# Kernel optimization log

Measured on AMD Instinct MI355X. Metric: run time of the kernel, lower is better.

Reference implementation:

```python
import jax, jax.numpy as jnp
import numpy as np

B, T, N, F = 16, 12, 1024, 128
H, DH, C = 8, 16, 64  # heads, d_head (=d_core//H), core_num; note d_in must equal H*DH
EPS = 1e-5


def setup_inputs() -> dict:
    key = jax.random.key(0)
    ks = jax.random.split(key, 12)
    s = lambda fan_in: 1.0 / np.sqrt(fan_in)
    return {
        "input": jax.random.normal(ks[0], (B, T, N, F), jnp.float32),
        # value Linear(d_in,d_in); weights stored [in,out]
        "W_v": jax.random.normal(ks[1], (F, F), jnp.float32) * s(F),
        "b_v": jax.random.normal(ks[2], (F,), jnp.float32) * s(F),
        # core decomposition params
        "adaptive": jax.random.normal(ks[3], (H, DH, N), jnp.float32),
        "cores": jax.random.normal(ks[4], (H, C, DH), jnp.float32),
        # FFN: Linear(2F -> 8F), GELU, Linear(8F -> F)
        "W1": jax.random.normal(ks[5], (2 * F, 8 * F), jnp.float32) * s(2 * F),
        "b1": jax.random.normal(ks[6], (8 * F,), jnp.float32) * s(2 * F),
        "W2": jax.random.normal(ks[7], (8 * F, F), jnp.float32) * s(8 * F),
        "b2": jax.random.normal(ks[8], (F,), jnp.float32) * s(8 * F),
        # BatchNorm2d(d_in) affine params (training-mode batch stats)
        "gamma": jnp.ones((F,), jnp.float32),
        "beta": jnp.zeros((F,), jnp.float32),
    }


def reference(input, W_v, b_v, adaptive, cores, W1, b1, W2, b2, gamma, beta):
    b, t, n, f = input.shape
    h, dh, _ = adaptive.shape
    # value projection, split heads: [b,t,n,f] -> [b,t,h,dh,n]
    v = input @ W_v + b_v
    v = v.reshape(b, t, n, h, dh).transpose(0, 1, 3, 4, 2)
    # core affinity scores [h,c,n]
    aff = jnp.einsum("hcd,hdn->hcn", cores, adaptive) / np.sqrt(dh)
    a_n2c = jax.nn.softmax(aff, axis=-1)  # softmax over nodes
    a_c2n = jax.nn.softmax(aff, axis=-2)  # softmax over cores
    # two-stage aggregation through cores
    v = jnp.einsum("bthfn,hcn->bthfc", v, a_n2c)
    v = jnp.einsum("bthfc,hcn->bthfn", v, a_c2n)
    # merge heads: [b,t,h,dh,n] -> [b,t,f,n] -> [b,t,n,f]
    v = v.reshape(b, t, f, n).swapaxes(-1, -2)
    # FFN on concat([input - v, v]) (dropout off in eval), residual
    x = jnp.concatenate([input - v, v], axis=-1)
    x = jax.nn.gelu(x @ W1 + b1, approximate=False) @ W2 + b2
    out = x + input
    # BatchNorm2d over channel f (batch stats over b,t,n; biased variance)
    mean = out.mean(axis=(0, 1, 2))
    var = out.var(axis=(0, 1, 2))
    return (out - mean) * jax.lax.rsqrt(var + EPS) * gamma + beta
```

## Files before the change

kernel.cpp:

```cpp
#include <hip/hip_runtime.h>
#include <math.h>

#define BB 16
#define TT 12
#define NN 1024
#define FF 128
#define BT 192
#define BTN 196608
#define CNT ((float)BTN)
#define T1SZ 1572864

typedef unsigned short ushort_t;
typedef __attribute__((ext_vector_type(8))) short bf16x8;
typedef __attribute__((ext_vector_type(4))) float f32x4;

__device__ __forceinline__ ushort_t f2bf(float x) {
    union { float f; unsigned u; } c; c.f = x;
    unsigned r = c.u + 0x7fffu + ((c.u >> 16) & 1u);
    return (ushort_t)(r >> 16);
}
__device__ __forceinline__ float bf2f(ushort_t u) {
    union { unsigned u32; float f; } c; c.u32 = ((unsigned)u) << 16; return c.f;
}
__device__ __forceinline__ unsigned pk2(float a, float b) {
    unsigned r;
    asm("v_cvt_pk_bf16_f32 %0, %1, %2" : "=v"(r) : "v"(a), "v"(b));
    return r;
}
__device__ __forceinline__ float gelu_f(float x) {
    float u = x * x;
    float s = x * fmaf(u, -0.10294428f, -2.30220852f);
    float e = __builtin_amdgcn_exp2f(s);
    return x * __builtin_amdgcn_rcpf(1.0f + e);
}

__device__ __forceinline__ char* swz256(void* base, int row, int byteoff) {
    return (char*)base + row * 256 + (byteoff ^ ((row & 7) << 4));
}

__global__ __launch_bounds__(256) void k_sm_n(const float* __restrict__ cores,
                                              const float* __restrict__ adaptive,
                                              float* __restrict__ aff,
                                              ushort_t* __restrict__ out) {
    int row = blockIdx.x;
    int h = row >> 6;
    int t = threadIdx.x;
    __shared__ float red[8];
    const float* cp = cores + row * 16;
    const float* ap = adaptive + h * 16384;
    float v0 = 0.f, v1 = 0.f, v2 = 0.f, v3 = 0.f;
#pragma unroll
    for (int d = 0; d < 16; ++d) {
        float c = cp[d];
        const float* an = ap + d * 1024;
        v0 = fmaf(c, an[t], v0);
        v1 = fmaf(c, an[t + 256], v1);
        v2 = fmaf(c, an[t + 512], v2);
        v3 = fmaf(c, an[t + 768], v3);
    }
    v0 *= 0.25f; v1 *= 0.25f; v2 *= 0.25f; v3 *= 0.25f;
    aff[row * 1024 + t]       = v0;
    aff[row * 1024 + t + 256] = v1;
    aff[row * 1024 + t + 512] = v2;
    aff[row * 1024 + t + 768] = v3;
    float m = fmaxf(fmaxf(v0, v1), fmaxf(v2, v3));
#pragma unroll
    for (int off = 32; off >= 1; off >>= 1) m = fmaxf(m, __shfl_xor(m, off));
    if ((t & 63) == 0) red[t >> 6] = m;
    __syncthreads();
    m = fmaxf(fmaxf(red[0], red[1]), fmaxf(red[2], red[3]));
    v0 = expf(v0 - m); v1 = expf(v1 - m); v2 = expf(v2 - m); v3 = expf(v3 - m);
    float s = v0 + v1 + v2 + v3;
#pragma unroll
    for (int off = 32; off >= 1; off >>= 1) s += __shfl_xor(s, off);
    __syncthreads();
    if ((t & 63) == 0) red[4 + (t >> 6)] = s;
    __syncthreads();
    s = red[4] + red[5] + red[6] + red[7];
    float inv = 1.0f / s;
    out[row * 1024 + t]       = f2bf(v0 * inv);
    out[row * 1024 + t + 256] = f2bf(v1 * inv);
    out[row * 1024 + t + 512] = f2bf(v2 * inv);
    out[row * 1024 + t + 768] = f2bf(v3 * inv);
}

__global__ __launch_bounds__(256) void k_prep(const float* __restrict__ aff,
                                              const float* __restrict__ Wv,
                                              const float* __restrict__ W1,
                                              const float* __restrict__ W2,
                                              ushort_t* __restrict__ a_c2nT,
                                              ushort_t* __restrict__ WvT,
                                              ushort_t* __restrict__ W1f,
                                              ushort_t* __restrict__ W2f,
                                              float* __restrict__ bn_sum) {
    __shared__ __align__(16) char smem[64 * 65 * 4];
    int b = blockIdx.x;
    int t = threadIdx.x;
    if (b < 128) {
        ushort_t (*tile)[72] = (ushort_t(*)[72])smem;
        int h = b >> 4, n0 = (b & 15) * 64;
        int nl = t >> 2, q = t & 3;
        const float* p = aff + h * 65536 + n0 + nl;
        float v[16];
        float m = -1e30f;
#pragma unroll
        for (int i = 0; i < 16; ++i) {
            v[i] = p[(q * 16 + i) * 1024];
            m = fmaxf(m, v[i]);
        }
        m = fmaxf(m, __shfl_xor(m, 1));
        m = fmaxf(m, __shfl_xor(m, 2));
        float s = 0.f;
#pragma unroll
        for (int i = 0; i < 16; ++i) { v[i] = expf(v[i] - m); s += v[i]; }
        s += __shfl_xor(s, 1);
        s += __shfl_xor(s, 2);
        float inv = 1.0f / s;
#pragma unroll
        for (int i = 0; i < 16; ++i) tile[nl][q * 16 + i] = f2bf(v[i] * inv);
        __syncthreads();
        ushort_t* ob = a_c2nT + ((size_t)h * 1024 + n0) * 64;
        for (int i = t; i < 512; i += 256) {
            int r = i >> 3, cq = i & 7;
            *(bf16x8*)&ob[r * 64 + cq * 8] = *(bf16x8*)&tile[r][cq * 8];
        }
    } else if (b < 132) {
        float (*tile)[65] = (float(*)[65])smem;
        int q = b - 128;
        int r0 = (q >> 1) * 64, c0 = (q & 1) * 64;
        for (int i = t; i < 4096; i += 256) {
            int r = i >> 6, c = i & 63;
            tile[r][c] = Wv[(size_t)(r0 + r) * 128 + c0 + c];
        }
        __syncthreads();
        for (int i = t; i < 4096; i += 256) {
            int c = i >> 6, r = i & 63;
            WvT[(size_t)(c0 + c) * 128 + r0 + r] = f2bf(tile[r][c]);
        }
    } else if (b < 260) {
        int tid = (b - 132) * 256 + t;
        int lane = tid & 63, jn = (tid >> 6) & 1, kk = (tid >> 7) & 7;
        int w = (tid >> 10) & 3, ch = tid >> 12;
        int lr = lane & 15, lg = lane >> 4;
        int n = ch * 128 + w * 32 + jn * 16 + lr;
        int kb = kk * 32 + lg * 8;
        ushort_t o[8];
#pragma unroll
        for (int e = 0; e < 8; ++e) o[e] = f2bf(W1[(size_t)(kb + e) * 1024 + n]);
        *(bf16x8*)&W1f[(size_t)tid * 8] = *(bf16x8*)o;
    } else if (b < 324) {
        int tid = (b - 260) * 256 + t;
        int lane = tid & 63, jy = (tid >> 6) & 1, kk = (tid >> 7) & 3;
        int w = (tid >> 9) & 3, ch = tid >> 11;
        int lr = lane & 15, lg = lane >> 4;
        int f = w * 32 + jy * 16 + lr;
        int kb = ch * 128 + kk * 32 + lg * 8;
        ushort_t o[8];
#pragma unroll
        for (int e = 0; e < 8; ++e) o[e] = f2bf(W2[(size_t)(kb + e) * 128 + f]);
        *(bf16x8*)&W2f[(size_t)tid * 8] = *(bf16x8*)o;
    } else {
        bn_sum[t] = 0.f;
    }
}

__global__ __launch_bounds__(256) void k_vs1(const float* __restrict__ input,
                                             const ushort_t* __restrict__ WvT,
                                             const float* __restrict__ bv,
                                             const ushort_t* __restrict__ a_n2c,
                                             float* __restrict__ T1p) {
    __shared__ __align__(16) ushort_t as_lds[128 * 128];
    __shared__ __align__(16) ushort_t vsT[128 * 128];
    int bt = blockIdx.x;
    int part = blockIdx.y;
    int t = threadIdx.x, w = t >> 6, lane = t & 63, lr = lane & 15, lg = lane >> 4;

    f32x4 t1acc[2][4];
#pragma unroll
    for (int hl = 0; hl < 2; ++hl)
#pragma unroll
        for (int mi = 0; mi < 4; ++mi) t1acc[hl][mi] = (f32x4){0.f, 0.f, 0.f, 0.f};

    for (int c8 = part * 2; c8 < part * 2 + 2; ++c8) {
        int n0 = c8 * 128;
        __syncthreads();
        for (int j = 0; j < 16; ++j) {
            int i = j * 256 + t;
            int r = i >> 5, cq = i & 31;
            float4 f = *(const float4*)&input[((size_t)(bt * 1024 + n0 + r)) * 128 + cq * 4];
            uint2 o;
            o.x = pk2(f.x, f.y);
            o.y = pk2(f.z, f.w);
            *(uint2*)swz256(as_lds, r, cq * 8) = o;
        }
        __syncthreads();
        f32x4 vacc[2][8];
#pragma unroll
        for (int mi = 0; mi < 2; ++mi)
#pragma unroll
            for (int jn = 0; jn < 8; ++jn) {
                float bb = bv[jn * 16 + lr];
                vacc[mi][jn] = (f32x4){bb, bb, bb, bb};
            }
#pragma unroll
        for (int ks = 0; ks < 4; ++ks) {
            bf16x8 a[2];
#pragma unroll
            for (int mi = 0; mi < 2; ++mi)
                a[mi] = *(const bf16x8*)swz256(as_lds, w * 32 + mi * 16 + lr, ks * 64 + lg * 16);
#pragma unroll
            for (int jn = 0; jn < 8; ++jn) {
                bf16x8 bfr = *(const bf16x8*)&WvT[(size_t)(jn * 16 + lr) * 128 + ks * 32 + lg * 8];
#pragma unroll
                for (int mi = 0; mi < 2; ++mi)
                    vacc[mi][jn] = __builtin_amdgcn_mfma_f32_16x16x32_bf16(a[mi], bfr, vacc[mi][jn], 0, 0, 0);
            }
        }
#pragma unroll
        for (int mi = 0; mi < 2; ++mi)
#pragma unroll
            for (int jn = 0; jn < 8; ++jn) {
                uint2 o;
                o.x = pk2(vacc[mi][jn][0], vacc[mi][jn][1]);
                o.y = pk2(vacc[mi][jn][2], vacc[mi][jn][3]);
                *(uint2*)swz256(vsT, jn * 16 + lr, w * 64 + mi * 32 + lg * 8) = o;
            }
        __syncthreads();
#pragma unroll
        for (int hl = 0; hl < 2; ++hl) {
            int h = w * 2 + hl;
#pragma unroll
            for (int ks = 0; ks < 4; ++ks) {
                bf16x8 bfr = *(const bf16x8*)swz256(vsT, h * 16 + lr, ks * 64 + lg * 16);
#pragma unroll
                for (int mi = 0; mi < 4; ++mi) {
                    bf16x8 a = *(const bf16x8*)&a_n2c[((size_t)(h * 64 + mi * 16 + lr)) * 1024 + n0 + ks * 32 + lg * 8];
                    t1acc[hl][mi] = __builtin_amdgcn_mfma_f32_16x16x32_bf16(a, bfr, t1acc[hl][mi], 0, 0, 0);
                }
            }
        }
    }
    float* op = T1p + (size_t)part * T1SZ;
#pragma unroll
    for (int hl = 0; hl < 2; ++hl) {
        int h = w * 2 + hl;
#pragma unroll
        for (int mi = 0; mi < 4; ++mi)
            *(f32x4*)&op[(((size_t)bt * 8 + h) * 16 + lr) * 64 + mi * 16 + lg * 4] = t1acc[hl][mi];
    }
}

__global__ __launch_bounds__(256) void k_t1conv(const float* __restrict__ T1p,
                                                ushort_t* __restrict__ T1t) {
    size_t i4 = ((size_t)blockIdx.x * 256 + threadIdx.x) * 4;
    float4 s = *(const float4*)&T1p[i4];
#pragma unroll
    for (int p = 1; p < 4; ++p) {
        float4 v = *(const float4*)&T1p[(size_t)p * T1SZ + i4];
        s.x += v.x; s.y += v.y; s.z += v.z; s.w += v.w;
    }
    uint2 o;
    o.x = pk2(s.x, s.y);
    o.y = pk2(s.z, s.w);
    *(uint2*)&T1t[i4] = o;
}

__global__ __launch_bounds__(256) void k_ffn(
        const float* __restrict__ input,
        const ushort_t* __restrict__ a_c2nT,
        const ushort_t* __restrict__ T1t,
        const ushort_t* __restrict__ W1f,
        const ushort_t* __restrict__ W2f,
        const float* __restrict__ b1,
        const float* __restrict__ b2,
        float* __restrict__ out,
        float* __restrict__ bn_sum,
        float* __restrict__ bn_sq) {
    __shared__ __align__(16) ushort_t x2mb[4 * 8 * 64 * 8];
    __shared__ __align__(16) ushort_t hmb[4 * 4 * 64 * 8];
    int bt = blockIdx.y;
    int n0 = blockIdx.x * 64;
    int t = threadIdx.x;
    int w = t >> 6, lane = t & 63, lr = lane & 15, lg = lane >> 4;
    int R0 = w * 16;
    int rowbase = bt * 1024 + n0;

    {
        const ushort_t* tp = T1t + ((size_t)(bt * 128) + lr) * 64 + lg * 8;
        const ushort_t* ap = a_c2nT + ((size_t)(n0 + R0 + lr)) * 64 + lg * 8;
        ushort_t* mb = x2mb + w * 4096;
        int wbase = ((lg >> 1) * 16 + lr) * 8 + (lg & 1) * 4;
#pragma unroll
        for (int h = 0; h < 8; ++h) {
            f32x4 vacc = {0.f, 0.f, 0.f, 0.f};
#pragma unroll
            for (int kk = 0; kk < 2; ++kk) {
                bf16x8 af = *(const bf16x8*)(tp + h * 1024 + kk * 32);
                bf16x8 bf = *(const bf16x8*)(ap + (size_t)h * 65536 + kk * 32);
                vacc = __builtin_amdgcn_mfma_f32_16x16x32_bf16(af, bf, vacc, 0, 0, 0);
            }
            float4 inp = *(const float4*)&input[(size_t)(rowbase + R0 + lr) * 128 + h * 16 + lg * 4];
            uint2 lft, rgt;
            lft.x = pk2(inp.x - vacc[0], inp.y - vacc[1]);
            lft.y = pk2(inp.z - vacc[2], inp.w - vacc[3]);
            rgt.x = pk2(vacc[0], vacc[1]);
            rgt.y = pk2(vacc[2], vacc[3]);
            *(uint2*)&mb[wbase + h * 256]         = lft;
            *(uint2*)&mb[wbase + (h + 8) * 256]   = rgt;
        }
    }
    __syncthreads();

    f32x4 yacc[4][2];
#pragma unroll
    for (int mi = 0; mi < 4; ++mi)
#pragma unroll
        for (int jy = 0; jy < 2; ++jy) {
            float bb = b2[w * 32 + jy * 16 + lr];
            yacc[mi][jy] = (f32x4){bb, bb, bb, bb};
        }

    int hwbase = w * 2048 + ((lg >> 1) * 16 + lr) * 8 + (lg & 1) * 4;

#define GEMM1_INTO(HACC, CH) {                                                        \
        _Pragma("unroll")                                                             \
        for (int jn = 0; jn < 2; ++jn) {                                              \
            f32x4 bb = *(const f32x4*)&b1[(CH) * 128 + w * 32 + jn * 16 + lg * 4];    \
            _Pragma("unroll")                                                         \
            for (int mi = 0; mi < 4; ++mi) HACC[jn][mi] = bb;                         \
        }                                                                             \
        const ushort_t* w1p = W1f + ((size_t)((CH) * 4 + w) * 16) * 512 + lane * 8;   \
        __builtin_amdgcn_s_setprio(1);                                                \
        _Pragma("unroll")                                                             \
        for (int kk = 0; kk < 8; ++kk) {                                              \
            bf16x8 xf[4];                                                             \
            _Pragma("unroll")                                                         \
            for (int mi = 0; mi < 4; ++mi)                                            \
                xf[mi] = *(const bf16x8*)&x2mb[mi * 4096 + kk * 512 + lane * 8];      \
            _Pragma("unroll")                                                         \
            for (int jn = 0; jn < 2; ++jn) {                                          \
                bf16x8 wf = *(const bf16x8*)(w1p + (kk * 2 + jn) * 512);              \
                _Pragma("unroll")                                                     \
                for (int mi = 0; mi < 4; ++mi)                                        \
                    HACC[jn][mi] = __builtin_amdgcn_mfma_f32_16x16x32_bf16(wf, xf[mi], HACC[jn][mi], 0, 0, 0); \
            }                                                                         \
        }                                                                             \
        __builtin_amdgcn_s_setprio(0);                                                \
    }

#define GELU_STORE(HACC) {                                                            \
        _Pragma("unroll")                                                             \
        for (int jn = 0; jn < 2; ++jn)                                                \
            _Pragma("unroll")                                                         \
            for (int mi = 0; mi < 4; ++mi) {                                          \
                uint2 o;                                                              \
                o.x = pk2(gelu_f(HACC[jn][mi][0]), gelu_f(HACC[jn][mi][1]));          \
                o.y = pk2(gelu_f(HACC[jn][mi][2]), gelu_f(HACC[jn][mi][3]));          \
                *(uint2*)&hmb[hwbase + jn * 256 + mi * 512] = o;                      \
            }                                                                         \
    }

#define GEMM2_CHUNK(CH) {                                                             \
        bf16x8 b2r[4][2];                                                             \
        const ushort_t* w2p = W2f + (((size_t)((CH) * 4 + w) * 4) * 2) * 512 + lane * 8; \
        _Pragma("unroll")                                                             \
        for (int kk = 0; kk < 4; ++kk)                                                \
            _Pragma("unroll")                                                         \
            for (int jy = 0; jy < 2; ++jy)                                            \
                b2r[kk][jy] = *(const bf16x8*)(w2p + (kk * 2 + jy) * 512);            \
        __builtin_amdgcn_s_setprio(1);                                                \
        _Pragma("unroll")                                                             \
        for (int kk = 0; kk < 4; ++kk) {                                              \
            bf16x8 a4[4];                                                             \
            _Pragma("unroll")                                                         \
            for (int mi = 0; mi < 4; ++mi)                                            \
                a4[mi] = *(const bf16x8*)&hmb[kk * 2048 + mi * 512 + lane * 8];       \
            _Pragma("unroll")                                                         \
            for (int jy = 0; jy < 2; ++jy)                                            \
                _Pragma("unroll")                                                     \
                for (int mi = 0; mi < 4; ++mi)                                        \
                    yacc[mi][jy] = __builtin_amdgcn_mfma_f32_16x16x32_bf16(a4[mi], b2r[kk][jy], yacc[mi][jy], 0, 0, 0); \
        }                                                                             \
        __builtin_amdgcn_s_setprio(0);                                                \
    }

    f32x4 haccA[2][4], haccB[2][4];
    GEMM1_INTO(haccA, 0);
#pragma unroll
    for (int cc = 0; cc < 4; ++cc) {
        int ch = cc * 2;
        __syncthreads();
        GELU_STORE(haccA);
        __syncthreads();
        GEMM1_INTO(haccB, ch + 1);
        GEMM2_CHUNK(ch);
        __syncthreads();
        GELU_STORE(haccB);
        __syncthreads();
        if (cc < 3) GEMM1_INTO(haccA, ch + 2);
        GEMM2_CHUNK(ch + 1);
    }
#undef GEMM1_INTO
#undef GELU_STORE
#undef GEMM2_CHUNK

    float sacc[2] = {0.f, 0.f}, qacc[2] = {0.f, 0.f};
#pragma unroll
    for (int mi = 0; mi < 4; ++mi)
#pragma unroll
        for (int jy = 0; jy < 2; ++jy)
#pragma unroll
            for (int r = 0; r < 4; ++r) {
                int gr = rowbase + mi * 16 + lg * 4 + r;
                int gc = w * 32 + jy * 16 + lr;
                float val = yacc[mi][jy][r] + input[(size_t)gr * 128 + gc];
                out[(size_t)gr * 128 + gc] = val;
                sacc[jy] += val;
                qacc[jy] += val * val;
            }
#pragma unroll
    for (int jy = 0; jy < 2; ++jy) {
        float s = sacc[jy], q = qacc[jy];
        s += __shfl_xor(s, 16); s += __shfl_xor(s, 32);
        q += __shfl_xor(q, 16); q += __shfl_xor(q, 32);
        if (lg == 0) {
            atomicAdd(&bn_sum[w * 32 + jy * 16 + lr], s);
            atomicAdd(&bn_sq[w * 32 + jy * 16 + lr], q);
        }
    }
}

__global__ __launch_bounds__(256) void k_bnapply(float* __restrict__ out,
                                                 const float* __restrict__ bn_sum,
                                                 const float* __restrict__ bn_sq,
                                                 const float* __restrict__ gamma,
                                                 const float* __restrict__ beta) {
    size_t idx = (size_t)blockIdx.x * 256 + threadIdx.x;
    int c = (int)((idx * 4) & 127);
    float4 v = *(float4*)&out[idx * 4];
    float4 sm = *(const float4*)&bn_sum[c];
    float4 sq = *(const float4*)&bn_sq[c];
    float4 gm = *(const float4*)&gamma[c];
    float4 bt = *(const float4*)&beta[c];
    const float inv = 1.0f / CNT;
    float4 sc, sh;
#pragma unroll
    for (int j = 0; j < 4; ++j) {
        float mean = ((const float*)&sm)[j] * inv;
        float var  = ((const float*)&sq)[j] * inv - mean * mean;
        float s = ((const float*)&gm)[j] * rsqrtf(var + 1e-5f);
        ((float*)&sc)[j] = s;
        ((float*)&sh)[j] = ((const float*)&bt)[j] - mean * s;
    }
    v.x = fmaf(v.x, sc.x, sh.x);
    v.y = fmaf(v.y, sc.y, sh.y);
    v.z = fmaf(v.z, sc.z, sh.z);
    v.w = fmaf(v.w, sc.w, sh.w);
    *(float4*)&out[idx * 4] = v;
}

extern "C" void kernel_launch(void* const* d_in, const int* in_sizes, int n_in,
                              void* d_out, int out_size, void* d_ws, size_t ws_size,
                              hipStream_t stream) {
    const float* input    = (const float*)d_in[0];
    const float* Wv       = (const float*)d_in[1];
    const float* bv       = (const float*)d_in[2];
    const float* adaptive = (const float*)d_in[3];
    const float* cores    = (const float*)d_in[4];
    const float* W1       = (const float*)d_in[5];
    const float* b1       = (const float*)d_in[6];
    const float* W2       = (const float*)d_in[7];
    const float* b2       = (const float*)d_in[8];
    const float* gamma    = (const float*)d_in[9];
    const float* beta     = (const float*)d_in[10];
    float* out = (float*)d_out;
    float* ws  = (float*)d_ws;

    float*    aff    = ws;
    ushort_t* a_n2c  = (ushort_t*)(ws + 524288);
    ushort_t* a_c2nT = (ushort_t*)(ws + 786432);
    ushort_t* T1t    = (ushort_t*)(ws + 1048576);
    ushort_t* W1f    = (ushort_t*)(ws + 1835008);
    ushort_t* W2f    = (ushort_t*)(ws + 1966080);
    ushort_t* WvT    = (ushort_t*)(ws + 2031616);
    float* bn_sum    = ws + 2039808;
    float* bn_sq     = bn_sum + 128;
    float* T1p       = ws + 2097152;

    k_sm_n   <<<512, 256, 0, stream>>>(cores, adaptive, aff, a_n2c);
    k_prep   <<<325, 256, 0, stream>>>(aff, Wv, W1, W2, a_c2nT, WvT, W1f, W2f, bn_sum);
    k_vs1    <<<dim3(BT, 4), 256, 0, stream>>>(input, WvT, bv, a_n2c, T1p);
    k_t1conv <<<1536, 256, 0, stream>>>(T1p, T1t);
    k_ffn    <<<dim3(16, BT), 256, 0, stream>>>(input, a_c2nT, T1t, W1f, W2f,
                                                b1, b2, out, bn_sum, bn_sq);
    k_bnapply<<<(out_size / 4) / 256, 256, 0, stream>>>(out, bn_sum, bn_sq, gamma, beta);
}
```

Before: 387.3 us.

## Split FFN work per wave over row-halves and hidden-halves, removing block barriers

Reorganizes the FFN kernel so each wave owns 32 rows and half of each hidden chunk. Each wave keeps its GELU output in a private LDS slice, so the per-chunk __syncthreads and the double-buffered accumulator scheme go away. W1/W2 prepacking is reordered to match the new fragment order. Each wave now accumulates partial sums for all 128 output features, and wave pairs exchange and add these partials through LDS at the end. The cost is twice the output accumulator registers, reduced x-fragment reuse, and an extra reduction step.

```diff
diff --git a/kernel.cpp b/kernel.cpp
--- a/kernel.cpp
+++ b/kernel.cpp
@@ -139,10 +139,10 @@
         }
     } else if (b < 260) {
         int tid = (b - 132) * 256 + t;
-        int lane = tid & 63, jn = (tid >> 6) & 1, kk = (tid >> 7) & 7;
-        int w = (tid >> 10) & 3, ch = tid >> 12;
+        int lane = tid & 63, jn = (tid >> 6) & 3, kk = (tid >> 8) & 7;
+        int hh = (tid >> 11) & 1, ch = tid >> 12;
         int lr = lane & 15, lg = lane >> 4;
-        int n = ch * 128 + w * 32 + jn * 16 + lr;
+        int n = ch * 128 + hh * 64 + jn * 16 + lr;
         int kb = kk * 32 + lg * 8;
         ushort_t o[8];
 #pragma unroll
@@ -150,11 +150,11 @@
         *(bf16x8*)&W1f[(size_t)tid * 8] = *(bf16x8*)o;
     } else if (b < 324) {
         int tid = (b - 260) * 256 + t;
-        int lane = tid & 63, jy = (tid >> 6) & 1, kk = (tid >> 7) & 3;
-        int w = (tid >> 9) & 3, ch = tid >> 11;
+        int lane = tid & 63, jf = (tid >> 6) & 7, ks = (tid >> 9) & 1;
+        int hh = (tid >> 10) & 1, ch = tid >> 11;
         int lr = lane & 15, lg = lane >> 4;
-        int f = w * 32 + jy * 16 + lr;
-        int kb = ch * 128 + kk * 32 + lg * 8;
+        int f = jf * 16 + lr;
+        int kb = ch * 128 + hh * 64 + ks * 32 + lg * 8;
         ushort_t o[8];
 #pragma unroll
         for (int e = 0; e < 8; ++e) o[e] = f2bf(W2[(size_t)(kb + e) * 128 + f]);
@@ -277,11 +277,12 @@
         float* __restrict__ bn_sum,
         float* __restrict__ bn_sq) {
     __shared__ __align__(16) ushort_t x2mb[4 * 8 * 64 * 8];
-    __shared__ __align__(16) ushort_t hmb[4 * 4 * 64 * 8];
+    __shared__ __align__(16) ushort_t gmb[4 * 2 * 16 * 72];
     int bt = blockIdx.y;
     int n0 = blockIdx.x * 64;
     int t = threadIdx.x;
     int w = t >> 6, lane = t & 63, lr = lane & 15, lg = lane >> 4;
+    int th = w >> 1, hh = w & 1;
     int R0 = w * 16;
     int rowbase = bt * 1024 + n0;
 
@@ -311,121 +312,120 @@
     }
     __syncthreads();
 
-    f32x4 yacc[4][2];
-#pragma unroll
-    for (int mi = 0; mi < 4; ++mi)
-#pragma unroll
-        for (int jy = 0; jy < 2; ++jy) {
-            float bb = b2[w * 32 + jy * 16 + lr];
-            yacc[mi][jy] = (f32x4){bb, bb, bb, bb};
-        }
-
-    int hwbase = w * 2048 + ((lg >> 1) * 16 + lr) * 8 + (lg & 1) * 4;
-
-#define GEMM1_INTO(HACC, CH) {                                                        \
-        _Pragma("unroll")                                                             \
-        for (int jn = 0; jn < 2; ++jn) {                                              \
-            f32x4 bb = *(const f32x4*)&b1[(CH) * 128 + w * 32 + jn * 16 + lg * 4];    \
-            _Pragma("unroll")                                                         \
-            for (int mi = 0; mi < 4; ++mi) HACC[jn][mi] = bb;                         \
-        }                                                                             \
-        const ushort_t* w1p = W1f + ((size_t)((CH) * 4 + w) * 16) * 512 + lane * 8;   \
-        __builtin_amdgcn_s_setprio(1);                                                \
-        _Pragma("unroll")                                                             \
-        for (int kk = 0; kk < 8; ++kk) {                                              \
-            bf16x8 xf[4];                                                             \
-            _Pragma("unroll")                                                         \
-            for (int mi = 0; mi < 4; ++mi)                                            \
-                xf[mi] = *(const bf16x8*)&x2mb[mi * 4096 + kk * 512 + lane * 8];      \
-            _Pragma("unroll")                                                         \
-            for (int jn = 0; jn < 2; ++jn) {                                          \
-                bf16x8 wf = *(const bf16x8*)(w1p + (kk * 2 + jn) * 512);              \
-                _Pragma("unroll")                                                     \
-                for (int mi = 0; mi < 4; ++mi)                                        \
-                    HACC[jn][mi] = __builtin_amdgcn_mfma_f32_16x16x32_bf16(wf, xf[mi], HACC[jn][mi], 0, 0, 0); \
-            }                                                                         \
-        }                                                                             \
-        __builtin_amdgcn_s_setprio(0);                                                \
-    }
-
-#define GELU_STORE(HACC) {                                                            \
-        _Pragma("unroll")                                                             \
-        for (int jn = 0; jn < 2; ++jn)                                                \
-            _Pragma("unroll")                                                         \
-            for (int mi = 0; mi < 4; ++mi) {                                          \
-                uint2 o;                                                              \
-                o.x = pk2(gelu_f(HACC[jn][mi][0]), gelu_f(HACC[jn][mi][1]));          \
-                o.y = pk2(gelu_f(HACC[jn][mi][2]), gelu_f(HACC[jn][mi][3]));          \
-                *(uint2*)&hmb[hwbase + jn * 256 + mi * 512] = o;                      \
-            }                                                                         \
-    }
-
-#define GEMM2_CHUNK(CH) {                                                             \
-        bf16x8 b2r[4][2];                                                             \
-        const ushort_t* w2p = W2f + (((size_t)((CH) * 4 + w) * 4) * 2) * 512 + lane * 8; \
-        _Pragma("unroll")                                                             \
-        for (int kk = 0; kk < 4; ++kk)                                                \
-            _Pragma("unroll")                                                         \
-            for (int jy = 0; jy < 2; ++jy)                                            \
-                b2r[kk][jy] = *(const bf16x8*)(w2p + (kk * 2 + jy) * 512);            \
-        __builtin_amdgcn_s_setprio(1);                                                \
-        _Pragma("unroll")                                                             \
-        for (int kk = 0; kk < 4; ++kk) {                                              \
-            bf16x8 a4[4];                                                             \
-            _Pragma("unroll")                                                         \
-            for (int mi = 0; mi < 4; ++mi)                                            \
-                a4[mi] = *(const bf16x8*)&hmb[kk * 2048 + mi * 512 + lane * 8];       \
-            _Pragma("unroll")                                                         \
-            for (int jy = 0; jy < 2; ++jy)                                            \
-                _Pragma("unroll")                                                     \
-                for (int mi = 0; mi < 4; ++mi)                                        \
-                    yacc[mi][jy] = __builtin_amdgcn_mfma_f32_16x16x32_bf16(a4[mi], b2r[kk][jy], yacc[mi][jy], 0, 0, 0); \
-        }                                                                             \
-        __builtin_amdgcn_s_setprio(0);                                                \
-    }
-
-    f32x4 haccA[2][4], haccB[2][4];
-    GEMM1_INTO(haccA, 0);
-#pragma unroll
-    for (int cc = 0; cc < 4; ++cc) {
-        int ch = cc * 2;
-        __syncthreads();
-        GELU_STORE(haccA);
-        __syncthreads();
-        GEMM1_INTO(haccB, ch + 1);
-        GEMM2_CHUNK(ch);
-        __syncthreads();
-        GELU_STORE(haccB);
-        __syncthreads();
-        if (cc < 3) GEMM1_INTO(haccA, ch + 2);
-        GEMM2_CHUNK(ch + 1);
-    }
-#undef GEMM1_INTO
-#undef GELU_STORE
-#undef GEMM2_CHUNK
-
-    float sacc[2] = {0.f, 0.f}, qacc[2] = {0.f, 0.f};
-#pragma unroll
-    for (int mi = 0; mi < 4; ++mi)
-#pragma unroll
-        for (int jy = 0; jy < 2; ++jy)
+    f32x4 yacc[2][8];
+#pragma unroll
+    for (int mi = 0; mi < 2; ++mi)
+#pragma unroll
+        for (int jf = 0; jf < 8; ++jf) yacc[mi][jf] = (f32x4){0.f, 0.f, 0.f, 0.f};
+
+    ushort_t* gw = gmb + w * 2304;
+
+    for (int ch = 0; ch < 8; ++ch) {
+        f32x4 hacc[4][2];
+#pragma unroll
+        for (int jn = 0; jn < 4; ++jn) {
+            f32x4 bb = *(const f32x4*)&b1[ch * 128 + hh * 64 + jn * 16 + lg * 4];
+#pragma unroll
+            for (int mi = 0; mi < 2; ++mi) hacc[jn][mi] = bb;
+        }
+        const ushort_t* w1p = W1f + ((size_t)(ch * 2 + hh) * 32) * 512 + lane * 8;
+        __builtin_amdgcn_s_setprio(1);
+#pragma unroll
+        for (int kk = 0; kk < 8; ++kk) {
+            bf16x8 xf[2];
+#pragma unroll
+            for (int mi = 0; mi < 2; ++mi)
+                xf[mi] = *(const bf16x8*)&x2mb[(th * 2 + mi) * 4096 + kk * 512 + lane * 8];
+#pragma unroll
+            for (int jn = 0; jn < 4; ++jn) {
+                bf16x8 wf = *(const bf16x8*)(w1p + (kk * 4 + jn) * 512);
+#pragma unroll
+                for (int mi = 0; mi < 2; ++mi)
+                    hacc[jn][mi] = __builtin_amdgcn_mfma_f32_16x16x32_bf16(wf, xf[mi], hacc[jn][mi], 0, 0, 0);
+            }
+        }
+        __builtin_amdgcn_s_setprio(0);
+#pragma unroll
+        for (int jn = 0; jn < 4; ++jn)
+#pragma unroll
+            for (int mi = 0; mi < 2; ++mi) {
+                uint2 o;
+                o.x = pk2(gelu_f(hacc[jn][mi][0]), gelu_f(hacc[jn][mi][1]));
+                o.y = pk2(gelu_f(hacc[jn][mi][2]), gelu_f(hacc[jn][mi][3]));
+                *(uint2*)&gw[mi * 1152 + lr * 72 + jn * 16 + lg * 4] = o;
+            }
+        const ushort_t* w2p = W2f + ((size_t)((ch * 2 + hh) * 2) * 8) * 512 + lane * 8;
+        __builtin_amdgcn_s_setprio(1);
+#pragma unroll
+        for (int ks = 0; ks < 2; ++ks) {
+            bf16x8 af[2];
+#pragma unroll
+            for (int mi = 0; mi < 2; ++mi)
+                af[mi] = *(const bf16x8*)&gw[mi * 1152 + lr * 72 + ks * 32 + lg * 8];
+#pragma unroll
+            for (int jf = 0; jf < 8; ++jf) {
+                bf16x8 wf = *(const bf16x8*)(w2p + (ks * 8 + jf) * 512);
+#pragma unroll
+                for (int mi = 0; mi < 2; ++mi)
+                    yacc[mi][jf] = __builtin_amdgcn_mfma_f32_16x16x32_bf16(af[mi], wf, yacc[mi][jf], 0, 0, 0);
+            }
+        }
+        __builtin_amdgcn_s_setprio(0);
+    }
+
+    __syncthreads();
+    float* xch = (float*)x2mb;
+    {
+        int swz = 4 * (lg ^ (lr & 3));
+#pragma unroll
+        for (int mi = 0; mi < 2; ++mi)
+#pragma unroll
+            for (int jfl = 0; jfl < 4; ++jfl) {
+                int jf = (1 - hh) * 4 + jfl;
+                float* dst = xch + (((w * 2 + mi) * 4 + jfl) * 16 + lr) * 16;
+                *(f32x4*)&dst[swz] = yacc[mi][jf];
+            }
+    }
+    __syncthreads();
+    {
+        int swz = 4 * (lg ^ (lr & 3));
+#pragma unroll
+        for (int mi = 0; mi < 2; ++mi)
+#pragma unroll
+            for (int jfl = 0; jfl < 4; ++jfl) {
+                int jf = hh * 4 + jfl;
+                const float* src = xch + ((((w ^ 1) * 2 + mi) * 4 + jfl) * 16 + lr) * 16;
+                f32x4 p = *(const f32x4*)&src[swz];
+                yacc[mi][jf][0] += p[0]; yacc[mi][jf][1] += p[1];
+                yacc[mi][jf][2] += p[2]; yacc[mi][jf][3] += p[3];
+            }
+    }
+
+    float sacc[4] = {0.f, 0.f, 0.f, 0.f}, qacc[4] = {0.f, 0.f, 0.f, 0.f};
+#pragma unroll
+    for (int mi = 0; mi < 2; ++mi)
+#pragma unroll
+        for (int jfl = 0; jfl < 4; ++jfl) {
+            int jf = hh * 4 + jfl;
+            int f = jf * 16 + lr;
+            float bb = b2[f];
 #pragma unroll
             for (int r = 0; r < 4; ++r) {
-                int gr = rowbase + mi * 16 + lg * 4 + r;
-                int gc = w * 32 + jy * 16 + lr;
-                float val = yacc[mi][jy][r] + input[(size_t)gr * 128 + gc];
-                out[(size_t)gr * 128 + gc] = val;
-                sacc[jy] += val;
-                qacc[jy] += val * val;
-            }
-#pragma unroll
-    for (int jy = 0; jy < 2; ++jy) {
-        float s = sacc[jy], q = qacc[jy];
+                int gr = rowbase + th * 32 + mi * 16 + lg * 4 + r;
+                float val = yacc[mi][jf][r] + bb + input[(size_t)gr * 128 + f];
+                out[(size_t)gr * 128 + f] = val;
+                sacc[jfl] += val;
+                qacc[jfl] += val * val;
+            }
+        }
+#pragma unroll
+    for (int jfl = 0; jfl < 4; ++jfl) {
+        float s = sacc[jfl], q = qacc[jfl];
         s += __shfl_xor(s, 16); s += __shfl_xor(s, 32);
         q += __shfl_xor(q, 16); q += __shfl_xor(q, 32);
         if (lg == 0) {
-            atomicAdd(&bn_sum[w * 32 + jy * 16 + lr], s);
-            atomicAdd(&bn_sq[w * 32 + jy * 16 + lr], q);
+            atomicAdd(&bn_sum[hh * 64 + jfl * 16 + lr], s);
+            atomicAdd(&bn_sq[hh * 64 + jfl * 16 + lr], q);
         }
     }
 }
```

New measurement: 678.3 us. +75.2%, slower.
